# Performance work log

Measured on AMD Instinct MI355X. Metric: run time of the kernel, lower is better.

Reference implementation:

```python
import jax, jax.numpy as jnp
import numpy as np
from jax.scipy.linalg import expm

B, T, DIM = 8, 4096, 256


def setup_inputs() -> dict:
    key = jax.random.key(0)
    k1, k2 = jax.random.split(key)
    psi = jax.random.normal(k1, (B, T, 4, DIM), dtype=jnp.float32)
    H = jax.random.normal(k2, (4, DIM, DIM), dtype=jnp.float32) * 0.02
    return {"psi": psi, "H": H}


def reference(psi, H):
    # H_complex = H[0] + i*H[1]; components H[2], H[3] are unused (as in the torch code)
    H_complex = (H[0] + 1j * H[1]).astype(jnp.complex64)
    # Unitary-like evolution operator U = expm(-i * H_complex), [dim, dim] complex64
    U = expm(-1j * H_complex)
    # All 4 quaternion components share the same U -> one batched complex matmul
    psi_c = psi.astype(jnp.complex64)  # [B, T, 4, dim]
    evolved = jnp.einsum('btcd,de->btce', psi_c, U)  # complex matmul over last dim
    # Torch code keeps only the real part of each evolved component
    return evolved.real.astype(jnp.float32)
```

## Files before the change

kernel.cpp:

```cpp
#include <hip/hip_runtime.h>
#include <hip/hip_bf16.h>

#define NDIM 256
#define NN (NDIM*NDIM)

typedef __attribute__((ext_vector_type(8))) short s8bf;
typedef __attribute__((ext_vector_type(4))) float f32x4;

__device__ __forceinline__ unsigned short f2bf(float f) {
    union { float f; unsigned u; } v; v.f = f;
    unsigned u = v.u;
    return (unsigned short)((u + 0x7FFFu + ((u >> 16) & 1u)) >> 16);
}
__device__ __forceinline__ short f2bfs(float f) {
    __hip_bfloat16 h = __float2bfloat16(f);
    union { __hip_bfloat16 h; short s; } v; v.h = h;
    return v.s;
}

__global__ __launch_bounds__(1024) void kmm(
    const float* __restrict__ H, float2* __restrict__ M2c, float2* __restrict__ M3c,
    unsigned short* __restrict__ Ut, int mode) {
    __shared__ float2 As[16][257];
    __shared__ float2 Bs[256][17];
    __shared__ float2 Rs[3][16][17];
    const int tx = threadIdx.x, ty = threadIdx.y, tz = threadIdx.z;
    const int tid = (tz * 16 + ty) * 16 + tx;
    const int r0 = blockIdx.y * 16, c0 = blockIdx.x * 16;

#pragma unroll
    for (int i = 0; i < 4; ++i) {
        int idx = i * 1024 + tid;
        int r = idx >> 8, k = idx & 255;
        float2 a;
        if (mode == 0)      { a.x = H[NN + (r0+r)*NDIM + k]; a.y = -H[(r0+r)*NDIM + k]; }
        else if (mode == 1) a = M2c[(r0+r)*NDIM + k];
        else                a = M3c[(r0+r)*NDIM + k];
        As[r][k] = a;
    }
#pragma unroll
    for (int i = 0; i < 4; ++i) {
        int idx = i * 1024 + tid;
        int k = idx >> 4, cc = idx & 15;
        float2 b;
        if (mode <= 1) { b.x = H[NN + k*NDIM + c0+cc]; b.y = -H[k*NDIM + c0+cc]; }
        else {
            int g = k * NDIM + c0 + cc;
            float mr = H[NN + g], mi = -H[g];
            float2 m2 = M2c[g], m3 = M3c[g];
            float di = (k == c0 + cc) ? 1.f : 0.f;
            b.x = di*(1.f/6.f) + mr*(1.f/24.f) + m2.x*(1.f/120.f) + m3.x*(1.f/720.f);
            b.y =                mi*(1.f/24.f) + m2.y*(1.f/120.f) + m3.y*(1.f/720.f);
        }
        Bs[k][cc] = b;
    }
    __syncthreads();

    float sr0=0.f, si0=0.f, sr1=0.f, si1=0.f;
#pragma unroll 8
    for (int k = tz*64; k < tz*64 + 64; k += 2) {
        float2 a = As[ty][k], b = Bs[k][tx];
        sr0 = fmaf(a.x, b.x, sr0); sr0 = fmaf(-a.y, b.y, sr0);
        si0 = fmaf(a.x, b.y, si0); si0 = fmaf(a.y, b.x, si0);
        float2 a1 = As[ty][k+1], b1 = Bs[k+1][tx];
        sr1 = fmaf(a1.x, b1.x, sr1); sr1 = fmaf(-a1.y, b1.y, sr1);
        si1 = fmaf(a1.x, b1.y, si1); si1 = fmaf(a1.y, b1.x, si1);
    }
    float sr = sr0 + sr1, si = si0 + si1;
    if (tz > 0) Rs[tz-1][ty][tx] = make_float2(sr, si);
    __syncthreads();
    if (tz == 0) {
        sr += Rs[0][ty][tx].x + Rs[1][ty][tx].x + Rs[2][ty][tx].x;
        si += Rs[0][ty][tx].y + Rs[1][ty][tx].y + Rs[2][ty][tx].y;
        int d = r0 + ty, e = c0 + tx;
        if (mode == 0)      M2c[d*NDIM + e] = make_float2(sr, si);
        else if (mode == 1) M3c[d*NDIM + e] = make_float2(sr, si);
        else {
            int g = d * NDIM + e;
            float ur = sr + ((d == e) ? 1.f : 0.f) + H[NN + g] + M2c[g].x * 0.5f;
            Ut[e * NDIM + d] = f2bf(ur);
        }
    }
}

__global__ __launch_bounds__(1024, 4) void kgemm(
    const float* __restrict__ psi, const unsigned short* __restrict__ Ut,
    float* __restrict__ out) {
    __shared__ unsigned short Bls[NN];
    __shared__ float Escr[16][512];
    const int t = threadIdx.x;

    const s8bf* Ug = (const s8bf*)Ut;
    s8bf* Bg = (s8bf*)Bls;
#pragma unroll
    for (int i = 0; i < 8; ++i) {
        int g = i * 1024 + t;
        int r = g >> 5, j = g & 31;
        Bg[(r << 5) | (j ^ (r & 7))] = Ug[g];
    }
    __syncthreads();

    const int w = t >> 6, lane = t & 63;
    const int c = lane & 15, q = lane >> 4;
    const f32x4* psi4 = (const f32x4*)psi;
    f32x4* out4 = (f32x4*)out;
    float* Ebase = &Escr[w][0];

#pragma unroll 1
    for (int st = 0; st < 2; ++st) {
        const int base = blockIdx.x * 512 + st * 256 + w * 16;
        const size_t rl = (size_t)(base + c) * 64;

        f32x4 acc[16];
#pragma unroll
        for (int i = 0; i < 16; ++i) acc[i] = (f32x4)0.f;

        f32x4 pb[2][2];
        pb[0][0] = psi4[rl + q*2];     pb[0][1] = psi4[rl + q*2 + 1];
        pb[1][0] = psi4[rl + 8 + q*2]; pb[1][1] = psi4[rl + 8 + q*2 + 1];

#pragma unroll
        for (int s = 0; s < 8; ++s) {
            s8bf a;
#pragma unroll
            for (int j = 0; j < 4; ++j) {
                a[j]     = f2bfs(pb[s & 1][0][j]);
                a[j + 4] = f2bfs(pb[s & 1][1][j]);
            }
            if (s < 6) {
                int o = (s + 2) * 8 + q * 2;
                pb[s & 1][0] = psi4[rl + o];
                pb[s & 1][1] = psi4[rl + o + 1];
            }
#pragma unroll
            for (int ct = 0; ct < 16; ++ct) {
                int rr = ct * 16 + c;
                s8bf bb = Bg[(rr << 5) | ((s*4 + q) ^ (rr & 7))];
                acc[ct] = __builtin_amdgcn_mfma_f32_16x16x32_bf16(a, bb, acc[ct], 0, 0, 0);
            }
        }

#pragma unroll
        for (int p = 0; p < 16; ++p) {
            const int qq = p >> 2, rr = p & 3;
            float* E = Ebase + (p & 1) * 256;
            if (q == qq) {
#pragma unroll
                for (int ct = 0; ct < 16; ++ct)
                    E[ct * 16 + c] = acc[ct][rr];
            }
            f32x4 vv = *(const f32x4*)(&E[lane * 4]);
            __builtin_nontemporal_store(vv, &out4[(size_t)(base + p) * 64 + lane]);
            __builtin_amdgcn_sched_barrier(0);
        }
    }
}

extern "C" void kernel_launch(void* const* d_in, const int* in_sizes, int n_in,
                              void* d_out, int out_size, void* d_ws, size_t ws_size,
                              hipStream_t stream) {
    const float* psi = (const float*)d_in[0];
    const float* H   = (const float*)d_in[1];
    float* out = (float*)d_out;

    float2* M2c = (float2*)d_ws;
    float2* M3c = M2c + NN;
    unsigned short* Ut = (unsigned short*)(M3c + NN);

    dim3 cb(16, 16, 4), cg(16, 16);
    kmm<<<cg, cb, 0, stream>>>(H, M2c, M3c, Ut, 0);
    kmm<<<cg, cb, 0, stream>>>(H, M2c, M3c, Ut, 1);
    kmm<<<cg, cb, 0, stream>>>(H, M2c, M3c, Ut, 2);
    kgemm<<<256, 1024, 0, stream>>>(psi, Ut, out);
}
```

Before: 72.21 us.

## Hold U tiles in registers and switch GEMM to 32x32x16 MFMA

Result: slower. 116.7 us (+61.6%).

```diff
diff --git a/kernel.cpp b/kernel.cpp
--- a/kernel.cpp
+++ b/kernel.cpp
@@ -6,6 +6,7 @@
 
 typedef __attribute__((ext_vector_type(8))) short s8bf;
 typedef __attribute__((ext_vector_type(4))) float f32x4;
+typedef __attribute__((ext_vector_type(16))) float f32x16;
 
 __device__ __forceinline__ unsigned short f2bf(float f) {
     union { float f; unsigned u; } v; v.f = f;
@@ -83,75 +84,60 @@
     }
 }
 
-__global__ __launch_bounds__(1024, 4) void kgemm(
+__global__ __launch_bounds__(512, 2) void kgemm(
     const float* __restrict__ psi, const unsigned short* __restrict__ Ut,
     float* __restrict__ out) {
-    __shared__ unsigned short Bls[NN];
-    __shared__ float Escr[16][512];
     const int t = threadIdx.x;
+    const int w = t >> 6, l = t & 63;
+    const int lr = l & 31, half = l >> 5;
+    const int cg = w & 3, rg = w >> 2;
+    const int colb = cg * 64;
 
-    const s8bf* Ug = (const s8bf*)Ut;
-    s8bf* Bg = (s8bf*)Bls;
+    s8bf b0[16], b1[16];
 #pragma unroll
-    for (int i = 0; i < 8; ++i) {
-        int g = i * 1024 + t;
-        int r = g >> 5, j = g & 31;
-        Bg[(r << 5) | (j ^ (r & 7))] = Ug[g];
+    for (int ks = 0; ks < 16; ++ks) {
+        b0[ks] = *(const s8bf*)(&Ut[(colb +      lr) * NDIM + ks * 16 + half * 8]);
+        b1[ks] = *(const s8bf*)(&Ut[(colb + 32 + lr) * NDIM + ks * 16 + half * 8]);
     }
-    __syncthreads();
 
-    const int w = t >> 6, lane = t & 63;
-    const int c = lane & 15, q = lane >> 4;
     const f32x4* psi4 = (const f32x4*)psi;
-    f32x4* out4 = (f32x4*)out;
-    float* Ebase = &Escr[w][0];
+    const size_t rowL = (size_t)blockIdx.x * 256 + rg * 128 + lr;
 
-#pragma unroll 1
-    for (int st = 0; st < 2; ++st) {
-        const int base = blockIdx.x * 512 + st * 256 + w * 16;
-        const size_t rl = (size_t)(base + c) * 64;
+    f32x4 ring[4][2];
+#pragma unroll
+    for (int p = 0; p < 4; ++p) {
+        size_t ad = (rowL + (size_t)(p >> 4) * 32) * 64 + (p & 15) * 4 + half * 2;
+        ring[p][0] = psi4[ad]; ring[p][1] = psi4[ad + 1];
+    }
 
-        f32x4 acc[16];
-#pragma unroll
-        for (int i = 0; i < 16; ++i) acc[i] = (f32x4)0.f;
-
-        f32x4 pb[2][2];
-        pb[0][0] = psi4[rl + q*2];     pb[0][1] = psi4[rl + q*2 + 1];
-        pb[1][0] = psi4[rl + 8 + q*2]; pb[1][1] = psi4[rl + 8 + q*2 + 1];
+    f32x16 acc0 = (f32x16)0.f, acc1 = (f32x16)0.f;
 
 #pragma unroll
-        for (int s = 0; s < 8; ++s) {
-            s8bf a;
+    for (int p = 0; p < 64; ++p) {
+        const int ks = p & 15, strip = p >> 4;
+        s8bf a;
 #pragma unroll
-            for (int j = 0; j < 4; ++j) {
-                a[j]     = f2bfs(pb[s & 1][0][j]);
-                a[j + 4] = f2bfs(pb[s & 1][1][j]);
+        for (int j = 0; j < 4; ++j) {
+            a[j]     = f2bfs(ring[p & 3][0][j]);
+            a[j + 4] = f2bfs(ring[p & 3][1][j]);
+        }
+        if (p + 4 < 64) {
+            const int pn = p + 4;
+            size_t ad = (rowL + (size_t)(pn >> 4) * 32) * 64 + (pn & 15) * 4 + half * 2;
+            ring[p & 3][0] = psi4[ad]; ring[p & 3][1] = psi4[ad + 1];
+        }
+        acc0 = __builtin_amdgcn_mfma_f32_32x32x16_bf16(a, b0[ks], acc0, 0, 0, 0);
+        acc1 = __builtin_amdgcn_mfma_f32_32x32x16_bf16(a, b1[ks], acc1, 0, 0, 0);
+
+        if (ks == 15) {
+            const size_t r0 = (size_t)blockIdx.x * 256 + rg * 128 + strip * 32;
+#pragma unroll
+            for (int r = 0; r < 16; ++r) {
+                size_t row = r0 + (r & 3) + 8 * (r >> 2) + 4 * half;
+                __builtin_nontemporal_store(acc0[r], &out[row * NDIM + colb + lr]);
+                __builtin_nontemporal_store(acc1[r], &out[row * NDIM + colb + 32 + lr]);
             }
-            if (s < 6) {
-                int o = (s + 2) * 8 + q * 2;
-                pb[s & 1][0] = psi4[rl + o];
-                pb[s & 1][1] = psi4[rl + o + 1];
-            }
-#pragma unroll
-            for (int ct = 0; ct < 16; ++ct) {
-                int rr = ct * 16 + c;
-                s8bf bb = Bg[(rr << 5) | ((s*4 + q) ^ (rr & 7))];
-                acc[ct] = __builtin_amdgcn_mfma_f32_16x16x32_bf16(a, bb, acc[ct], 0, 0, 0);
-            }
-        }
-
-#pragma unroll
-        for (int p = 0; p < 16; ++p) {
-            const int qq = p >> 2, rr = p & 3;
-            float* E = Ebase + (p & 1) * 256;
-            if (q == qq) {
-#pragma unroll
-                for (int ct = 0; ct < 16; ++ct)
-                    E[ct * 16 + c] = acc[ct][rr];
-            }
-            f32x4 vv = *(const f32x4*)(&E[lane * 4]);
-            __builtin_nontemporal_store(vv, &out4[(size_t)(base + p) * 64 + lane]);
-            __builtin_amdgcn_sched_barrier(0);
+            acc0 = (f32x16)0.f; acc1 = (f32x16)0.f;
         }
     }
 }
@@ -171,5 +157,5 @@
     kmm<<<cg, cb, 0, stream>>>(H, M2c, M3c, Ut, 0);
     kmm<<<cg, cb, 0, stream>>>(H, M2c, M3c, Ut, 1);
     kmm<<<cg, cb, 0, stream>>>(H, M2c, M3c, Ut, 2);
-    kgemm<<<256, 1024, 0, stream>>>(psi, Ut, out);
+    kgemm<<<512, 512, 0, stream>>>(psi, Ut, out);
 }
```
